# Kernel optimization log

Hardware: AMD Instinct MI355X
Metric: run time of the kernel (lower is better)

The kernel has to match this reference:

```python
import jax, jax.numpy as jnp
import numpy as np
from functools import partial


@partial(jax.custom_vjp, nondiff_argnums=(1,))
def binarize1d(x, upper):
    return jnp.round(jnp.clip(x, 0.0, upper))

def _b1_fwd(x, upper):
    return jnp.round(jnp.clip(x, 0.0, upper)), x

def _b1_bwd(upper, x, g):
    # torch Binarize.backward for 1-D input: zero grad outside [0, upper]
    return (jnp.where((x < 0.0) | (x > upper), 0.0, g),)

binarize1d.defvjp(_b1_fwd, _b1_bwd)


def binarize2d(x, upper):
    # torch Binarize.backward for >=2-D input passes grad through unchanged -> STE
    return x + jax.lax.stop_gradient(jnp.round(jnp.clip(x, 0.0, upper)) - x)


def _perm_matrices(wc, wr, C, R):
    b = binarize1d(wc, float(C - 1))  # [C] selected row index per column
    # identity_column[i,j] = i  ->  col[i,j] = 1 iff i == b[j]
    col = binarize2d(1.0 - jnp.abs(jnp.arange(C, dtype=wc.dtype)[:, None] - b[None, :]), 1.0)
    r = binarize1d(wr, float(R - 1))  # [R] selected column index per row
    # identity_row[i,j] = j  ->  row[i,j] = 1 iff j == r[i]
    row = binarize2d(1.0 - jnp.abs(jnp.arange(R, dtype=wr.dtype)[None, :] - r[:, None]), 1.0)
    return col, row, b, r


def _fix_duplicates(sel, n):
    # sel: int32 [n]. Reassign every non-first occurrence of a value to an unused
    # slot. Deterministic stand-in for the original list + random.shuffle + pop():
    # unused slots are consumed in descending order (ascending list, pop from end).
    i = jnp.arange(n)
    eq = (sel[None, :] == sel[:, None]) & (i[:, None] < i[None, :])
    dup = eq.any(axis=0)  # dup[j]: sel[j] already seen at some earlier index
    counts = jnp.zeros((n,), jnp.int32).at[sel].add(1)
    empty_desc = jnp.sort(jnp.where(counts == 0, i, -1))[::-1]
    rank = jnp.cumsum(dup.astype(jnp.int32)) - 1
    return jnp.where(dup, empty_desc[rank], sel), dup


def _forward(x, weight_column, weight_row):
    C = weight_column.shape[0]
    R = weight_row.shape[0]
    # __update_rearrange_matrix__ : build selection indices from current weights
    _, _, b, r = _perm_matrices(weight_column, weight_row, C, R)
    bi = jax.lax.stop_gradient(b).astype(jnp.int32)
    ri = jax.lax.stop_gradient(r).astype(jnp.int32)
    # __constraint_rearrange_matrix__ : in-place .data rewrite of colliding entries
    new_b, dup_c = _fix_duplicates(bi, C)
    new_r, dup_r = _fix_duplicates(ri, R)
    wc = weight_column + jax.lax.stop_gradient(
        jnp.where(dup_c, new_b.astype(weight_column.dtype), weight_column) - weight_column)
    wr = weight_row + jax.lax.stop_gradient(
        jnp.where(dup_r, new_r.astype(weight_row.dtype), weight_row) - weight_row)
    # final __update_rearrange_matrix__ with the constrained weights
    col_mat, row_mat, _, _ = _perm_matrices(wc, wr, C, R)
    out = jnp.matmul(x, col_mat)    # [B, R, C] : column permutation
    out = jnp.matmul(row_mat, out)  # [B, R, C] : row permutation
    return out


def setup_inputs():
    key = jax.random.key(0)
    k1, k2, k3 = jax.random.split(key, 3)
    B, R, C = 16, 1024, 2048
    x = jax.random.normal(k1, (B, R, C), dtype=jnp.float32)
    weight_column = jax.random.uniform(k2, (C,), dtype=jnp.float32) * C  # uniform(0, C) as in reset_parameters
    weight_row = jax.random.uniform(k3, (R,), dtype=jnp.float32) * R
    return {"x": x, "weight_column": weight_column, "weight_row": weight_row}


def reference(x, weight_column, weight_row):
    return _forward(x, weight_column, weight_row)
```

## Files before the change

### kernel.cpp

```cpp
#include <hip/hip_runtime.h>

#define MAXN 2048

__global__ void build_map_kernel(const float* __restrict__ wc, const float* __restrict__ wr,
                                 int C, int R,
                                 int* __restrict__ colmap, int* __restrict__ rowmap) {
    const float* w;
    int n;
    int* outmap;
    if (blockIdx.x == 0) { w = wc; n = C; outmap = colmap; }
    else                 { w = wr; n = R; outmap = rowmap; }

    __shared__ int sel[MAXN];
    __shared__ int first[MAXN];
    __shared__ int emptyslot[MAXN];
    __shared__ int dts[256], ets[256];

    const int t = threadIdx.x;
    const int base = t * 8;
    const float upper = (float)(n - 1);

    for (int k = 0; k < 8; k++) {
        int idx = base + k;
        if (idx < n) {
            float v = w[idx];
            v = fminf(fmaxf(v, 0.0f), upper);
            sel[idx]   = (int)rintf(v);
            first[idx] = 0x7fffffff;
        }
    }
    __syncthreads();
    for (int k = 0; k < 8; k++) {
        int idx = base + k;
        if (idx < n) atomicMin(&first[sel[idx]], idx);
    }
    __syncthreads();

    int dflag[8], eflag[8];
    int dsum = 0, esum = 0;
    for (int k = 0; k < 8; k++) {
        int idx = base + k;
        if (idx < n) {
            dflag[k] = (first[sel[idx]] != idx) ? 1 : 0;
            eflag[k] = (first[idx] == 0x7fffffff) ? 1 : 0;
        } else { dflag[k] = 0; eflag[k] = 0; }
        dsum += dflag[k]; esum += eflag[k];
    }

    dts[t] = dsum; ets[t] = esum;
    __syncthreads();
    for (int off = 1; off < 256; off <<= 1) {
        int dv = 0, ev = 0;
        if (t >= off) { dv = dts[t - off]; ev = ets[t - off]; }
        __syncthreads();
        dts[t] += dv; ets[t] += ev;
        __syncthreads();
    }
    const int dexc = dts[t] - dsum;
    const int eexc = ets[t] - esum;
    const int E    = ets[255];

    int erun = eexc;
    for (int k = 0; k < 8; k++) {
        int idx = base + k;
        if (idx < n && eflag[k]) emptyslot[E - 1 - erun] = idx;
        erun += eflag[k];
    }
    __syncthreads();

    int drun = dexc;
    for (int k = 0; k < 8; k++) {
        int idx = base + k;
        if (idx < n) outmap[idx] = dflag[k] ? emptyslot[drun] : sel[idx];
        drun += dflag[k];
    }
}

__global__ __launch_bounds__(256) void gather_kernel(
        const float* __restrict__ x,
        const int* __restrict__ rowmap,
        const int* __restrict__ colmap,
        float* __restrict__ out,
        int R, int C, int total) {
    __shared__ float lds[4 * MAXN];
    const int wave = threadIdx.x >> 6;
    const int lane = threadIdx.x & 63;
    const int row = blockIdx.x * 4 + wave;
    if (row >= total) return;

    const int b = row / R;
    const int i = row - b * R;
    const int sr = rowmap[i];

    const float4* __restrict__ src4 = (const float4*)(x + ((size_t)b * R + sr) * (size_t)C);
    float4*       __restrict__ dst4 = (float4*)(out + (size_t)row * (size_t)C);
    const int4*   __restrict__ cmap4 = (const int4*)colmap;

    float* wlds = lds + wave * MAXN;
    const int n4 = C >> 2;

    float4 v[8];
    #pragma unroll
    for (int k = 0; k < 8; k++) {
        int idx = lane + 64 * k;
        if (idx < n4) v[k] = src4[idx];
    }
    #pragma unroll
    for (int k = 0; k < 8; k++) {
        int idx = lane + 64 * k;
        if (idx < n4) ((float4*)wlds)[idx] = v[k];
    }
    #pragma unroll
    for (int k = 0; k < 8; k++) {
        int idx = lane + 64 * k;
        if (idx < n4) {
            int4 c = cmap4[idx];
            float4 o;
            o.x = wlds[c.x]; o.y = wlds[c.y]; o.z = wlds[c.z]; o.w = wlds[c.w];
            dst4[idx] = o;
        }
    }
}

extern "C" void kernel_launch(void* const* d_in, const int* in_sizes, int n_in,
                              void* d_out, int out_size, void* d_ws, size_t ws_size,
                              hipStream_t stream) {
    const float* x  = (const float*)d_in[0];
    const float* wc = (const float*)d_in[1];
    const float* wr = (const float*)d_in[2];
    const int C = in_sizes[1];
    const int R = in_sizes[2];
    const int B = in_sizes[0] / (R * C);

    int* colmap = (int*)d_ws;
    int* rowmap = colmap + C;

    const int total = B * R;
    build_map_kernel<<<2, 256, 0, stream>>>(wc, wr, C, R, colmap, rowmap);
    gather_kernel<<<(total + 3) / 4, 256, 0, stream>>>(x, rowmap, colmap,
                                                       (float*)d_out, R, C, total);
}
```

Baseline: 275.9 us.

## Process multiple rows per wave with register prefetch of next source row

Each wave now handles four output rows instead of one. The global loads for the next permuted source row are issued into registers while the current row is gathered from LDS and written out. Blocks shrink to two waves, with half the LDS per block. The aim is to overlap global-memory latency with the LDS gather and stores. The trade-off is fewer waves in flight overall and more serialized work per wave.

```diff
diff --git a/kernel.cpp b/kernel.cpp
--- a/kernel.cpp
+++ b/kernel.cpp
@@ -1,6 +1,7 @@
 #include <hip/hip_runtime.h>
 
 #define MAXN 2048
+#define ROWS_PER_WAVE 4
 
 __global__ void build_map_kernel(const float* __restrict__ wc, const float* __restrict__ wr,
                                  int C, int R,
@@ -76,48 +77,67 @@
     }
 }
 
-__global__ __launch_bounds__(256) void gather_kernel(
+__global__ __launch_bounds__(128) void gather_kernel(
         const float* __restrict__ x,
         const int* __restrict__ rowmap,
         const int* __restrict__ colmap,
         float* __restrict__ out,
         int R, int C, int total) {
-    __shared__ float lds[4 * MAXN];
+    __shared__ float lds[2 * MAXN];
     const int wave = threadIdx.x >> 6;
     const int lane = threadIdx.x & 63;
-    const int row = blockIdx.x * 4 + wave;
-    if (row >= total) return;
+    float* wlds = lds + wave * MAXN;
+    const int wid  = blockIdx.x * 2 + wave;
+    const int row0 = wid * ROWS_PER_WAVE;
+    if (row0 >= total) return;
 
-    const int b = row / R;
-    const int i = row - b * R;
-    const int sr = rowmap[i];
-
-    const float4* __restrict__ src4 = (const float4*)(x + ((size_t)b * R + sr) * (size_t)C);
-    float4*       __restrict__ dst4 = (float4*)(out + (size_t)row * (size_t)C);
-    const int4*   __restrict__ cmap4 = (const int4*)colmap;
-
-    float* wlds = lds + wave * MAXN;
     const int n4 = C >> 2;
+    const int4* __restrict__ cmap4 = (const int4*)colmap;
 
     float4 v[8];
-    #pragma unroll
-    for (int k = 0; k < 8; k++) {
-        int idx = lane + 64 * k;
-        if (idx < n4) v[k] = src4[idx];
+    {
+        const int b = row0 / R, i = row0 - b * R;
+        const float4* __restrict__ src4 =
+            (const float4*)(x + ((size_t)b * R + rowmap[i]) * (size_t)C);
+        #pragma unroll
+        for (int k = 0; k < 8; k++) {
+            int idx = lane + 64 * k;
+            if (idx < n4) v[k] = src4[idx];
+        }
     }
-    #pragma unroll
-    for (int k = 0; k < 8; k++) {
-        int idx = lane + 64 * k;
-        if (idx < n4) ((float4*)wlds)[idx] = v[k];
-    }
-    #pragma unroll
-    for (int k = 0; k < 8; k++) {
-        int idx = lane + 64 * k;
-        if (idx < n4) {
-            int4 c = cmap4[idx];
-            float4 o;
-            o.x = wlds[c.x]; o.y = wlds[c.y]; o.z = wlds[c.z]; o.w = wlds[c.w];
-            dst4[idx] = o;
+
+    for (int r = 0; r < ROWS_PER_WAVE; r++) {
+        const int row = row0 + r;
+        if (row >= total) break;
+
+        #pragma unroll
+        for (int k = 0; k < 8; k++) {
+            int idx = lane + 64 * k;
+            if (idx < n4) ((float4*)wlds)[idx] = v[k];
+        }
+
+        if (r + 1 < ROWS_PER_WAVE && row + 1 < total) {
+            const int nrow = row + 1;
+            const int b = nrow / R, i = nrow - b * R;
+            const float4* __restrict__ src4 =
+                (const float4*)(x + ((size_t)b * R + rowmap[i]) * (size_t)C);
+            #pragma unroll
+            for (int k = 0; k < 8; k++) {
+                int idx = lane + 64 * k;
+                if (idx < n4) v[k] = src4[idx];
+            }
+        }
+
+        float4* __restrict__ dst4 = (float4*)(out + (size_t)row * (size_t)C);
+        #pragma unroll
+        for (int k = 0; k < 8; k++) {
+            int idx = lane + 64 * k;
+            if (idx < n4) {
+                int4 c = cmap4[idx];
+                float4 o;
+                o.x = wlds[c.x]; o.y = wlds[c.y]; o.z = wlds[c.z]; o.w = wlds[c.w];
+                dst4[idx] = o;
+            }
         }
     }
 }
@@ -136,7 +156,10 @@
     int* rowmap = colmap + C;
 
     const int total = B * R;
+    const int rows_per_block = 2 * ROWS_PER_WAVE;
+    const int nblocks = (total + rows_per_block - 1) / rows_per_block;
+
     build_map_kernel<<<2, 256, 0, stream>>>(wc, wr, C, R, colmap, rowmap);
-    gather_kernel<<<(total + 3) / 4, 256, 0, stream>>>(x, rowmap, colmap,
-                                                       (float*)d_out, R, C, total);
+    gather_kernel<<<nblocks, 128, 0, stream>>>(x, rowmap, colmap,
+                                               (float*)d_out, R, C, total);
 }
```

Result: no change. 279.1 us (+1.2%).
